# Performance work log

Hardware: AMD Instinct MI355X
Metric: run time of the kernel (lower is better)

Reference implementation:

```python
import jax, jax.numpy as jnp
import numpy as np
from jax import lax

B, C, DM, NL, NROI, HID, RHID, REMB = 2, 32, 64, 4, 90, 64, 64, 32
S = DM * DM * DM
EPS = 1e-5
DN = ('NCDHW', 'OIDHW', 'NCDHW')


def setup_inputs() -> dict:
    key = jax.random.key(0)
    ks = jax.random.split(key, 14)
    w = lambda k, shp, s=0.05: (jax.random.normal(k, shp, jnp.float32) * s)
    atlas = (jax.random.uniform(ks[1], (NROI, S)) < 0.1).astype(jnp.float32)
    return {
        'data': jax.random.normal(ks[0], (B, 1, DM, DM, DM), jnp.float32),
        'atlas_mask': atlas,
        'conv0_w': w(ks[2], (C, 1, 3, 3, 3), 0.2),
        'conv0_b': w(ks[3], (C,)),
        'convs_w': w(ks[4], (NL - 1, C, C, 3, 3, 3)),
        'convs_b': w(ks[5], (NL - 1, C)),
        'scale_w1': w(ks[6], (NROI, C, HID)),
        'scale_b1': w(ks[7], (NROI, HID)),
        'scale_w2': w(ks[8], (NROI, HID, C)),
        'scale_b2': w(ks[9], (NROI, C)),
        'proj_w1': w(ks[10], (NROI, C, RHID)),
        'proj_b1': w(ks[11], (NROI, RHID)),
        'proj_w2': w(ks[12], (NROI, RHID, REMB)),
        'proj_b2': w(ks[13], (NROI, REMB)),
    }


def _inorm(x):
    # InstanceNorm3d(affine=False): normalize per (batch, channel) over spatial dims
    m = jnp.mean(x, axis=(2, 3, 4), keepdims=True)
    v = jnp.var(x, axis=(2, 3, 4), keepdims=True)
    return (x - m) * lax.rsqrt(v + EPS)


def _conv(x, w, b):
    y = lax.conv_general_dilated(x, w, (1, 1, 1), 'SAME', dimension_numbers=DN)
    return y + b[None, :, None, None, None]


def reference(data, atlas_mask, conv0_w, conv0_b, convs_w, convs_b,
              scale_w1, scale_b1, scale_w2, scale_b2,
              proj_w1, proj_b1, proj_w2, proj_b2):
    x = jax.nn.relu(_inorm(_conv(data, conv0_w, conv0_b)))
    for i in range(NL - 1):  # fixed small layer loop
        x = jax.nn.relu(_inorm(_conv(x, convs_w[i], convs_b[i])))
    emb = x.reshape(B, C, S)                                  # (B,C,S)
    # (B,C,S) x (S,n_roi) -> (B,n_roi,C), normalized by ROI voxel count
    roi = jnp.einsum('bcs,rs->brc', emb, atlas_mask)
    roi = roi / atlas_mask.sum(axis=-1)[None, :, None]
    # per-ROI gated MLP experts, batched over the roi axis
    h = jax.nn.relu(jnp.einsum('brc,rch->brh', roi, scale_w1) + scale_b1[None])
    gate = jax.nn.sigmoid(jnp.einsum('brh,rhc->brc', h, scale_w2) + scale_b2[None])
    f = gate * roi
    p = jax.nn.relu(jnp.einsum('brc,rch->brh', f, proj_w1) + proj_b1[None])
    out = jnp.einsum('brh,rhe->bre', p, proj_w2) + proj_b2[None]
    return out  # (B, n_roi, roi_emb)
```

## Files before the change

### kernel.cpp

```cpp
#include <hip/hip_runtime.h>
#include <hip/hip_bf16.h>
#include <math.h>

#define S_TOT 262144
#define EPS_F 1e-5f
#define NPART 512
#define PLSTR 14416

typedef __attribute__((ext_vector_type(8))) short s16x8;
typedef __attribute__((ext_vector_type(4))) float f32x4;
typedef __attribute__((ext_vector_type(4))) unsigned u32x4;

__device__ __forceinline__ unsigned short f2bf(float f) {
    unsigned u = __builtin_bit_cast(unsigned, f);
    unsigned r = (u + 0x7FFFu + ((u >> 16) & 1u)) >> 16;
    return (unsigned short)r;
}
__device__ __forceinline__ float bf2f(unsigned short u) {
    return __builtin_bit_cast(float, ((unsigned)u) << 16);
}
__device__ __forceinline__ unsigned cvt_pk_bf16(float a, float b) {
    unsigned r;
    asm("v_cvt_pk_bf16_f32 %0, %1, %2" : "=v"(r) : "v"(a), "v"(b));
    return r;
}

__global__ __launch_bounds__(256)
void prep_w_k(const float* __restrict__ conv0_w, const float* __restrict__ convs_w,
              unsigned short* __restrict__ wpad, unsigned short* __restrict__ whp)
{
    int idx = blockIdx.x * 256 + threadIdx.x;
    if (idx < 2048) {
        int brow = idx >> 5, k = idx & 31;
        int cout = 2 * (brow & 15) + (brow >> 4);
        float wv = (k < 27) ? conv0_w[cout * 27 + k] : 0.f;
        unsigned short hi = f2bf(wv);
        unsigned short lo = f2bf(wv - bf2f(hi));
        wpad[brow * 32 + k]        = hi;
        wpad[1024 + brow * 32 + k] = lo;
        return;
    }
    int j = idx - 2048;
    if (j >= 3 * 27648) return;
    int layer = j / 27648 + 1;
    int rem   = j % 27648;
    int tap   = rem >> 10;
    int cout  = (rem >> 5) & 31;
    int cin   = rem & 31;
    float wv = convs_w[(((layer - 1) * 32 + cout) * 32 + cin) * 27 + tap];
    unsigned short hi = f2bf(wv);
    int brow = ((cout & 1) << 4) | (cout >> 1);
    whp[(size_t)(layer - 1) * 27648 + tap * 1024 + brow * 32 + cin] = hi;
}

__global__ __launch_bounds__(512, 2)
void conv0_k(const float* __restrict__ in, const unsigned short* __restrict__ w0,
             unsigned short* __restrict__ outb, float* __restrict__ raw_out)
{
    __shared__ unsigned short sc[1824];
    __shared__ float s_red[512];

    const int tid  = threadIdx.x;
    const int lane = tid & 63;
    const int wv   = tid >> 6;
    const int row  = lane & 15;
    const int g4   = lane >> 4;

    const int blk = blockIdx.x;
    const int b   = blk >> 8;
    const int t   = blk & 255;
    const int x0  = (t & 7) << 3;
    const int y0  = ((t >> 3) & 7) << 3;
    const int z0  = (t >> 6) << 4;

    for (int i = tid; i < 1800; i += 512) {
        int zz = i / 100, r2 = i - zz * 100, yy = r2 / 10, xx = r2 - yy * 10;
        int gz = z0 + zz - 1, gy = y0 + yy - 1, gx = x0 + xx - 1;
        float v = 0.f;
        if ((unsigned)gz < 64u && (unsigned)gy < 64u && (unsigned)gx < 64u)
            v = in[((size_t)b << 18) + (gz << 12) + (gy << 6) + gx];
        sc[i] = (unsigned short)cvt_pk_bf16(v, v);
    }
    __syncthreads();

    int dvox[8];
    #pragma unroll
    for (int j = 0; j < 8; ++j) {
        int tap = g4 * 8 + j;
        if (tap < 27) {
            int dz = tap / 9, r9 = tap - dz * 9, dy = r9 / 3, dx = r9 - dy * 3;
            dvox[j] = dz * 100 + dy * 10 + dx;
        } else dvox[j] = 0;
    }

    s16x8 wh0 = *(const s16x8*)(w0 + row * 32 + g4 * 8);
    s16x8 wh1 = *(const s16x8*)(w0 + (16 + row) * 32 + g4 * 8);
    s16x8 wl0 = *(const s16x8*)(w0 + 1024 + row * 32 + g4 * 8);
    s16x8 wl1 = *(const s16x8*)(w0 + 1024 + (16 + row) * 32 + g4 * 8);

    f32x4 acc[2][4][2] = {};
    #pragma unroll
    for (int pl = 0; pl < 2; ++pl) {
        #pragma unroll
        for (int f = 0; f < 4; ++f) {
            int vvx = f * 16 + row;
            int base = (2 * wv + pl) * 100 + (vvx >> 3) * 10 + (vvx & 7);
            s16x8 a;
            #pragma unroll
            for (int j = 0; j < 8; ++j) a[j] = (short)sc[base + dvox[j]];
            acc[pl][f][0] = __builtin_amdgcn_mfma_f32_16x16x32_bf16(a, wh0, acc[pl][f][0], 0, 0, 0);
            acc[pl][f][0] = __builtin_amdgcn_mfma_f32_16x16x32_bf16(a, wl0, acc[pl][f][0], 0, 0, 0);
            acc[pl][f][1] = __builtin_amdgcn_mfma_f32_16x16x32_bf16(a, wh1, acc[pl][f][1], 0, 0, 0);
            acc[pl][f][1] = __builtin_amdgcn_mfma_f32_16x16x32_bf16(a, wl1, acc[pl][f][1], 0, 0, 0);
        }
    }

    {
        float s0 = 0.f, ss0 = 0.f, s1 = 0.f, ss1 = 0.f;
        #pragma unroll
        for (int pl = 0; pl < 2; ++pl)
            #pragma unroll
            for (int f = 0; f < 4; ++f)
                #pragma unroll
                for (int q = 0; q < 4; ++q) {
                    float v0 = acc[pl][f][0][q], v1 = acc[pl][f][1][q];
                    s0 += v0; ss0 += v0 * v0; s1 += v1; ss1 += v1 * v1;
                }
        s0 += __shfl_xor(s0, 16); s0 += __shfl_xor(s0, 32);
        ss0 += __shfl_xor(ss0, 16); ss0 += __shfl_xor(ss0, 32);
        s1 += __shfl_xor(s1, 16); s1 += __shfl_xor(s1, 32);
        ss1 += __shfl_xor(ss1, 16); ss1 += __shfl_xor(ss1, 32);
        if (lane < 16) {
            s_red[(wv * 32 + 2 * row) * 2]         = s0;
            s_red[(wv * 32 + 2 * row) * 2 + 1]     = ss0;
            s_red[(wv * 32 + 2 * row + 1) * 2]     = s1;
            s_red[(wv * 32 + 2 * row + 1) * 2 + 1] = ss1;
        }
    }

    #pragma unroll
    for (int pl = 0; pl < 2; ++pl) {
        int zp = 2 * wv + pl;
        unsigned short* ob = outb
            + ((((size_t)b << 18) + ((size_t)(z0 + zp) << 12) + (y0 << 6) + x0) << 5)
            + (row << 1);
        #pragma unroll
        for (int f = 0; f < 4; ++f) {
            #pragma unroll
            for (int qq = 0; qq < 4; ++qq) {
                int u = g4 * 4 + qq;
                int yy = f * 2 + (u >> 3), xx = u & 7;
                unsigned pk = cvt_pk_bf16(acc[pl][f][0][qq], acc[pl][f][1][qq]);
                *(unsigned*)(ob + ((yy << 6) + xx) * 32) = pk;
            }
        }
    }

    __syncthreads();
    if (tid < 64) {
        int n = tid & 31, sel = tid >> 5;
        float tot = 0.f;
        #pragma unroll
        for (int w = 0; w < 8; ++w) tot += s_red[(w * 32 + n) * 2 + sel];
        atomicAdd(&raw_out[(b * 32 + n) * 2 + sel], tot);
    }
}

__global__ __launch_bounds__(1024, 4)
void conv_slab_k(const unsigned short* __restrict__ in, const unsigned short* __restrict__ whp_l,
                 const float* __restrict__ raw_in, unsigned short* __restrict__ outb,
                 float* __restrict__ raw_out)
{
    __shared__ unsigned short tile[4 * PLSTR];
    __shared__ float s_red[1024];

    const int tid  = threadIdx.x;
    const int lane = tid & 63;
    const int wv   = tid >> 6;
    const int zz   = wv >> 1;
    const int yh   = (wv & 1) << 2;
    const int row  = lane & 15;
    const int g4   = lane >> 4;
    const int g    = tid & 3;
    const int vox0 = tid >> 2;

    const int blk = blockIdx.x;
    const int b   = blk >> 8;
    const int t   = blk & 255;
    const int x0  = (t & 3) << 4;
    const int y0  = ((t >> 2) & 7) << 3;
    const int z0  = (t >> 5) << 3;

    {
        float rs[8], sh[8];
        #pragma unroll
        for (int j = 0; j < 8; ++j) {
            int c = b * 32 + g * 8 + j;
            float sm = raw_in[c * 2], sq = raw_in[c * 2 + 1];
            float mean = sm * (1.f / 262144.f);
            float var  = sq * (1.f / 262144.f) - mean * mean;
            float r = rsqrtf(var + EPS_F);
            rs[j] = r; sh[j] = -mean * r;
        }
        #pragma unroll 1
        for (int u = 0; u < 8; ++u) {
            int vox = vox0 + u * 256;
            if (vox >= 1800) break;
            int zp = vox / 180, r2 = vox - zp * 180, yy = r2 / 18, xx = r2 - yy * 18;
            int gz = z0 + zp - 1, gy = y0 + yy - 1, gx = x0 + xx - 1;
            u32x4 w = (u32x4)0;
            if ((unsigned)gz < 64u && (unsigned)gy < 64u && (unsigned)gx < 64u) {
                u32x4 rv = *(const u32x4*)(in
                    + ((((size_t)b << 18) + (gz << 12) + (gy << 6) + gx) << 5) + (g << 3));
                #pragma unroll
                for (int k = 0; k < 4; ++k) {
                    float ve = __builtin_bit_cast(float, rv[k] << 16);
                    float vo = __builtin_bit_cast(float, rv[k] & 0xFFFF0000u);
                    float ne = fmaxf(0.f, fmaf(ve, rs[2 * k],     sh[2 * k]));
                    float no = fmaxf(0.f, fmaf(vo, rs[2 * k + 1], sh[2 * k + 1]));
                    w[k] = cvt_pk_bf16(ne, no);
                }
            }
            *(u32x4*)&tile[g * PLSTR + (vox << 3)] = w;
        }
    }
    __syncthreads();

    f32x4 acc[4][2] = {};
    {
        const unsigned short* aplane = &tile[g4 * PLSTR];
        const unsigned short* wrow = whp_l + row * 32 + g4 * 8;

        #pragma unroll 1
        for (int dz = 0; dz < 3; ++dz) {
            #pragma unroll 1
            for (int dx = 0; dx < 3; ++dx) {
                const int base = (((zz + dz) * 180 + yh * 18 + row + dx) << 3);
                s16x8 a6[6];
                #pragma unroll
                for (int r6 = 0; r6 < 6; ++r6)
                    a6[r6] = *(const s16x8*)&aplane[base + r6 * 144];

                #pragma unroll
                for (int dy = 0; dy < 3; ++dy) {
                    const int tap = (dz * 3 + dy) * 3 + dx;
                    s16x8 w0v = *(const s16x8*)(wrow + tap * 1024);
                    s16x8 w1v = *(const s16x8*)(wrow + tap * 1024 + 512);
                    __builtin_amdgcn_s_setprio(1);
                    acc[0][0] = __builtin_amdgcn_mfma_f32_16x16x32_bf16(a6[dy],     w0v, acc[0][0], 0, 0, 0);
                    acc[1][0] = __builtin_amdgcn_mfma_f32_16x16x32_bf16(a6[dy + 1], w0v, acc[1][0], 0, 0, 0);
                    acc[2][0] = __builtin_amdgcn_mfma_f32_16x16x32_bf16(a6[dy + 2], w0v, acc[2][0], 0, 0, 0);
                    acc[3][0] = __builtin_amdgcn_mfma_f32_16x16x32_bf16(a6[dy + 3], w0v, acc[3][0], 0, 0, 0);
                    acc[0][1] = __builtin_amdgcn_mfma_f32_16x16x32_bf16(a6[dy],     w1v, acc[0][1], 0, 0, 0);
                    acc[1][1] = __builtin_amdgcn_mfma_f32_16x16x32_bf16(a6[dy + 1], w1v, acc[1][1], 0, 0, 0);
                    acc[2][1] = __builtin_amdgcn_mfma_f32_16x16x32_bf16(a6[dy + 2], w1v, acc[2][1], 0, 0, 0);
                    acc[3][1] = __builtin_amdgcn_mfma_f32_16x16x32_bf16(a6[dy + 3], w1v, acc[3][1], 0, 0, 0);
                    __builtin_amdgcn_s_setprio(0);
                }
            }
        }
    }

    {
        float s0 = 0.f, ss0 = 0.f, s1 = 0.f, ss1 = 0.f;
        #pragma unroll
        for (int fr = 0; fr < 4; ++fr)
            #pragma unroll
            for (int q = 0; q < 4; ++q) {
                float v0 = acc[fr][0][q], v1 = acc[fr][1][q];
                s0 += v0; ss0 += v0 * v0; s1 += v1; ss1 += v1 * v1;
            }
        s0 += __shfl_xor(s0, 16); s0 += __shfl_xor(s0, 32);
        ss0 += __shfl_xor(ss0, 16); ss0 += __shfl_xor(ss0, 32);
        s1 += __shfl_xor(s1, 16); s1 += __shfl_xor(s1, 32);
        ss1 += __shfl_xor(ss1, 16); ss1 += __shfl_xor(ss1, 32);
        if (lane < 16) {
            s_red[(wv * 32 + 2 * row) * 2]         = s0;
            s_red[(wv * 32 + 2 * row) * 2 + 1]     = ss0;
            s_red[(wv * 32 + 2 * row + 1) * 2]     = s1;
            s_red[(wv * 32 + 2 * row + 1) * 2 + 1] = ss1;
        }
    }

    #pragma unroll
    for (int fr = 0; fr < 4; ++fr) {
        unsigned short* ob = outb
            + ((((size_t)b << 18) + ((size_t)(z0 + zz) << 12) + ((y0 + yh + fr) << 6) + x0) << 5)
            + (row << 1);
        #pragma unroll
        for (int qq = 0; qq < 4; ++qq) {
            unsigned pk = cvt_pk_bf16(acc[fr][0][qq], acc[fr][1][qq]);
            *(unsigned*)(ob + ((g4 * 4 + qq) << 5)) = pk;
        }
    }

    __syncthreads();
    if (tid < 64) {
        int n = tid & 31, sel = tid >> 5;
        float tot = 0.f;
        #pragma unroll
        for (int w = 0; w < 16; ++w) tot += s_red[(w * 32 + n) * 2 + sel];
        atomicAdd(&raw_out[(b * 32 + n) * 2 + sel], tot);
    }
}

__global__ __launch_bounds__(256)
void pool_mfma_k(const unsigned short* __restrict__ emb, const float* __restrict__ raw3,
                 const float* __restrict__ mask, float* __restrict__ part,
                 float* __restrict__ cntp)
{
    __shared__ unsigned short Ald[64 * 136];
    __shared__ unsigned short Bld[96 * 136];
    __shared__ float s_ns[128];

    const int tid  = threadIdx.x;
    const int lane = tid & 63, wv = tid >> 6;
    const int row  = lane & 15, g4 = lane >> 4;

    if (tid < 64) {
        float sm = raw3[tid * 2], sq = raw3[tid * 2 + 1];
        float mean = sm * (1.f / 262144.f);
        float var  = sq * (1.f / 262144.f) - mean * mean;
        float r = rsqrtf(var + EPS_F);
        s_ns[tid]      = r;
        s_ns[64 + tid] = -mean * r;
    }

    f32x4 acc[6] = {};
    float csum[6] = {};

    for (int ch = 0; ch < 4; ++ch) {
        const int s0 = (blockIdx.x * 4 + ch) << 7;
        __syncthreads();
        for (int i = tid; i < 1024; i += 256) {
            int bb = i >> 9, v = (i >> 2) & 127, g = i & 3;
            u32x4 rv = *(const u32x4*)(emb + (((size_t)bb << 18) + (size_t)(s0 + v)) * 32 + (g << 3));
            #pragma unroll
            for (int k = 0; k < 4; ++k) {
                int bc = bb * 32 + (g << 3) + 2 * k;
                float ve = __builtin_bit_cast(float, rv[k] << 16);
                float vo = __builtin_bit_cast(float, rv[k] & 0xFFFF0000u);
                float ne = fmaxf(0.f, fmaf(ve, s_ns[bc],     s_ns[64 + bc]));
                float no = fmaxf(0.f, fmaf(vo, s_ns[bc + 1], s_ns[64 + bc + 1]));
                unsigned pk = cvt_pk_bf16(ne, no);
                Ald[bc * 136 + v]       = (unsigned short)pk;
                Ald[(bc + 1) * 136 + v] = (unsigned short)(pk >> 16);
            }
        }
        #pragma unroll
        for (int k = 0; k < 6; ++k) {
            int i = tid + k * 256;
            int r = i >> 4, bs = i & 15;
            s16x8 vec = (s16x8)0;
            if (r < 90) {
                const float* mp = mask + (size_t)r * S_TOT + s0 + bs * 8;
                float4 m0 = *(const float4*)mp;
                float4 m1 = *(const float4*)(mp + 4);
                vec[0] = (m0.x != 0.f) ? (short)0x3F80 : (short)0;
                vec[1] = (m0.y != 0.f) ? (short)0x3F80 : (short)0;
                vec[2] = (m0.z != 0.f) ? (short)0x3F80 : (short)0;
                vec[3] = (m0.w != 0.f) ? (short)0x3F80 : (short)0;
                vec[4] = (m1.x != 0.f) ? (short)0x3F80 : (short)0;
                vec[5] = (m1.y != 0.f) ? (short)0x3F80 : (short)0;
                vec[6] = (m1.z != 0.f) ? (short)0x3F80 : (short)0;
                vec[7] = (m1.w != 0.f) ? (short)0x3F80 : (short)0;
                csum[k] += m0.x + m0.y + m0.z + m0.w + m1.x + m1.y + m1.z + m1.w;
            }
            *(s16x8*)&Bld[r * 136 + bs * 8] = vec;
        }
        __syncthreads();
        #pragma unroll
        for (int kk = 0; kk < 4; ++kk) {
            s16x8 a = *(const s16x8*)&Ald[(wv * 16 + row) * 136 + kk * 32 + g4 * 8];
            #pragma unroll
            for (int j = 0; j < 6; ++j) {
                s16x8 bb = *(const s16x8*)&Bld[(j * 16 + row) * 136 + kk * 32 + g4 * 8];
                acc[j] = __builtin_amdgcn_mfma_f32_16x16x32_bf16(a, bb, acc[j], 0, 0, 0);
            }
        }
    }
    #pragma unroll
    for (int k = 0; k < 6; ++k) {
        float c = csum[k];
        c += __shfl_xor(c, 1); c += __shfl_xor(c, 2);
        c += __shfl_xor(c, 4); c += __shfl_xor(c, 8);
        if ((tid & 15) == 0)
            cntp[(size_t)blockIdx.x * 96 + (tid >> 4) + k * 16] = c;
    }
    #pragma unroll
    for (int j = 0; j < 6; ++j) {
        *(f32x4*)&part[((size_t)blockIdx.x * 96 + j * 16 + row) * 64 + wv * 16 + g4 * 4]
            = acc[j];
    }
}

__global__ __launch_bounds__(256)
void mlp_k(const float* __restrict__ part, const float* __restrict__ cntp,
           const float* __restrict__ w1, const float* __restrict__ b1,
           const float* __restrict__ w2, const float* __restrict__ b2,
           const float* __restrict__ pw1, const float* __restrict__ pb1,
           const float* __restrict__ pw2, const float* __restrict__ pb2,
           float* __restrict__ out)
{
    const int r   = blockIdx.x % 90;
    const int b   = blockIdx.x / 90;
    const int tid = threadIdx.x;
    __shared__ float sred[8 * 32];
    __shared__ float scnt[4];
    __shared__ float roi_s[32], h_s[64], f_s[32], p_s[64];

    {
        float csp = 0.f;
        for (int p = tid; p < NPART; p += 256) csp += cntp[(size_t)p * 96 + r];
        #pragma unroll
        for (int off = 32; off > 0; off >>= 1) csp += __shfl_xor(csp, off);
        if ((tid & 63) == 0) scnt[tid >> 6] = csp;
    }
    {
        const int c = tid & 31, seg = tid >> 5;
        const float* pp = part + ((size_t)(seg * (NPART / 8)) * 96 + r) * 64 + b * 32 + c;
        float s = 0.f;
        #pragma unroll 4
        for (int p = 0; p < NPART / 8; ++p) s += pp[(size_t)p * 6144];
        sred[seg * 32 + c] = s;
    }
    __syncthreads();
    if (tid < 32) {
        float cs = scnt[0] + scnt[1] + scnt[2] + scnt[3];
        float t = 0.f;
        #pragma unroll
        for (int k = 0; k < 8; ++k) t += sred[k * 32 + tid];
        roi_s[tid] = t / cs;
    }
    __syncthreads();
    if (tid < 64) {
        float s = b1[r * 64 + tid];
        for (int c = 0; c < 32; ++c)
            s = fmaf(roi_s[c], w1[(r * 32 + c) * 64 + tid], s);
        h_s[tid] = fmaxf(s, 0.f);
    }
    __syncthreads();
    if (tid < 32) {
        float s = b2[r * 32 + tid];
        for (int j = 0; j < 64; ++j)
            s = fmaf(h_s[j], w2[(r * 64 + j) * 32 + tid], s);
        float gate = 1.f / (1.f + expf(-s));
        f_s[tid] = gate * roi_s[tid];
    }
    __syncthreads();
    if (tid < 64) {
        float s = pb1[r * 64 + tid];
        for (int c = 0; c < 32; ++c)
            s = fmaf(f_s[c], pw1[(r * 32 + c) * 64 + tid], s);
        p_s[tid] = fmaxf(s, 0.f);
    }
    __syncthreads();
    if (tid < 32) {
        float s = pb2[r * 32 + tid];
        for (int j = 0; j < 64; ++j)
            s = fmaf(p_s[j], pw2[(r * 64 + j) * 32 + tid], s);
        out[((size_t)b * 90 + r) * 32 + tid] = s;
    }
}

extern "C" void kernel_launch(void* const* d_in, const int* in_sizes, int n_in,
                              void* d_out, int out_size, void* d_ws, size_t ws_size,
                              hipStream_t stream)
{
    const float* data    = (const float*)d_in[0];
    const float* mask    = (const float*)d_in[1];
    const float* conv0_w = (const float*)d_in[2];
    const float* convs_w = (const float*)d_in[4];
    const float* sw1 = (const float*)d_in[6];
    const float* sb1 = (const float*)d_in[7];
    const float* sw2 = (const float*)d_in[8];
    const float* sb2 = (const float*)d_in[9];
    const float* pw1 = (const float*)d_in[10];
    const float* pb1 = (const float*)d_in[11];
    const float* pw2 = (const float*)d_in[12];
    const float* pb2 = (const float*)d_in[13];
    float* out = (float*)d_out;

    float* ws = (float*)d_ws;
    unsigned short* bufA = (unsigned short*)ws;
    unsigned short* bufB = (unsigned short*)(ws + 8388608);
    unsigned short* wpad = (unsigned short*)(ws + 16777216);
    unsigned short* whp  = (unsigned short*)(ws + 16887808);
    float* raw   = ws + 16929280;
    float* part  = ws + 17825792;
    float* cntp  = part + 3145728;

    hipMemsetAsync(raw, 0, 512 * sizeof(float), stream);
    prep_w_k<<<332, 256, 0, stream>>>(conv0_w, convs_w, wpad, whp);

    conv0_k<<<512, 512, 0, stream>>>(data, wpad, bufA, raw);
    conv_slab_k<<<512, 1024, 0, stream>>>(bufA, whp, raw, bufB, raw + 128);
    conv_slab_k<<<512, 1024, 0, stream>>>(bufB, whp + 27648, raw + 128, bufA, raw + 256);
    conv_slab_k<<<512, 1024, 0, stream>>>(bufA, whp + 2 * 27648, raw + 256, bufB, raw + 384);

    pool_mfma_k<<<NPART, 256, 0, stream>>>(bufB, raw + 384, mask, part, cntp);

    mlp_k<<<180, 256, 0, stream>>>(part, cntp, sw1, sb1, sw2, sb2,
                                   pw1, pb1, pw2, pb2, out);
}
```

Before: 214.2 us.

## Split conv slab into two double-buffered half tiles with load/compute overlap

Each conv block now processes two smaller 8x4x16 tiles instead of one 8x8x16 tile. The global loads for the second tile are issued into registers before the first tile's MFMA work and committed to a second LDS buffer afterwards. The goal is to hide global-load latency behind compute. The cost is a larger halo fraction, which means more redundant loads and LDS writes, plus fewer accumulators per wave and extra register pressure from the pending prefetch.

```diff
diff --git a/kernel.cpp b/kernel.cpp
--- a/kernel.cpp
+++ b/kernel.cpp
@@ -5,7 +5,7 @@
 #define S_TOT 262144
 #define EPS_F 1e-5f
 #define NPART 512
-#define PLSTR 14416
+#define PL    8656
 
 typedef __attribute__((ext_vector_type(8))) short s16x8;
 typedef __attribute__((ext_vector_type(4))) float f32x4;
@@ -167,18 +167,17 @@
 }
 
 __global__ __launch_bounds__(1024, 4)
-void conv_slab_k(const unsigned short* __restrict__ in, const unsigned short* __restrict__ whp_l,
+void conv_pipe_k(const unsigned short* __restrict__ in, const unsigned short* __restrict__ whp_l,
                  const float* __restrict__ raw_in, unsigned short* __restrict__ outb,
                  float* __restrict__ raw_out)
 {
-    __shared__ unsigned short tile[4 * PLSTR];
-    __shared__ float s_red[1024];
+    __shared__ unsigned short buf[2][4 * PL];
 
     const int tid  = threadIdx.x;
     const int lane = tid & 63;
     const int wv   = tid >> 6;
     const int zz   = wv >> 1;
-    const int yh   = (wv & 1) << 2;
+    const int yp   = (wv & 1) << 1;
     const int row  = lane & 15;
     const int g4   = lane >> 4;
     const int g    = tid & 3;
@@ -186,114 +185,134 @@
 
     const int blk = blockIdx.x;
     const int b   = blk >> 8;
-    const int t   = blk & 255;
-    const int x0  = (t & 3) << 4;
-    const int y0  = ((t >> 2) & 7) << 3;
-    const int z0  = (t >> 5) << 3;
-
-    {
-        float rs[8], sh[8];
-        #pragma unroll
-        for (int j = 0; j < 8; ++j) {
-            int c = b * 32 + g * 8 + j;
-            float sm = raw_in[c * 2], sq = raw_in[c * 2 + 1];
-            float mean = sm * (1.f / 262144.f);
-            float var  = sq * (1.f / 262144.f) - mean * mean;
-            float r = rsqrtf(var + EPS_F);
-            rs[j] = r; sh[j] = -mean * r;
-        }
-        #pragma unroll 1
-        for (int u = 0; u < 8; ++u) {
+    const int j   = blk & 255;
+
+    float rs[8], sh[8];
+    #pragma unroll
+    for (int k = 0; k < 8; ++k) {
+        int c = b * 32 + g * 8 + k;
+        float sm = raw_in[c * 2], sq = raw_in[c * 2 + 1];
+        float mean = sm * (1.f / 262144.f);
+        float var  = sq * (1.f / 262144.f) - mean * mean;
+        float r = rsqrtf(var + EPS_F);
+        rs[k] = r; sh[k] = -mean * r;
+    }
+
+    u32x4 pend[5];
+    int   okm = 0;
+
+    auto issue = [&](int t) {
+        int x0t = (t & 3) << 4, y0t = ((t >> 2) & 15) << 2, z0t = (t >> 6) << 3;
+        okm = 0;
+        #pragma unroll
+        for (int u = 0; u < 5; ++u) {
             int vox = vox0 + u * 256;
-            if (vox >= 1800) break;
-            int zp = vox / 180, r2 = vox - zp * 180, yy = r2 / 18, xx = r2 - yy * 18;
-            int gz = z0 + zp - 1, gy = y0 + yy - 1, gx = x0 + xx - 1;
+            int zp = vox / 108, r2 = vox - zp * 108, yy = r2 / 18, xx = r2 - yy * 18;
+            int gz = z0t + zp - 1, gy = y0t + yy - 1, gx = x0t + xx - 1;
+            bool ok = (vox < 1080) && ((unsigned)gz < 64u) && ((unsigned)gy < 64u)
+                      && ((unsigned)gx < 64u);
+            okm |= ((int)ok) << u;
+            u32x4 v = (u32x4)0;
+            if (ok)
+                v = *(const u32x4*)(in
+                    + ((((size_t)b << 18) + (gz << 12) + (gy << 6) + gx) << 5) + (g << 3));
+            pend[u] = v;
+        }
+    };
+
+    auto commit = [&](unsigned short* bp) {
+        #pragma unroll
+        for (int u = 0; u < 5; ++u) {
+            int vox = vox0 + u * 256;
+            if (vox >= 1080) continue;
             u32x4 w = (u32x4)0;
-            if ((unsigned)gz < 64u && (unsigned)gy < 64u && (unsigned)gx < 64u) {
-                u32x4 rv = *(const u32x4*)(in
-                    + ((((size_t)b << 18) + (gz << 12) + (gy << 6) + gx) << 5) + (g << 3));
+            if ((okm >> u) & 1) {
                 #pragma unroll
                 for (int k = 0; k < 4; ++k) {
-                    float ve = __builtin_bit_cast(float, rv[k] << 16);
-                    float vo = __builtin_bit_cast(float, rv[k] & 0xFFFF0000u);
+                    float ve = __builtin_bit_cast(float, pend[u][k] << 16);
+                    float vo = __builtin_bit_cast(float, pend[u][k] & 0xFFFF0000u);
                     float ne = fmaxf(0.f, fmaf(ve, rs[2 * k],     sh[2 * k]));
                     float no = fmaxf(0.f, fmaf(vo, rs[2 * k + 1], sh[2 * k + 1]));
                     w[k] = cvt_pk_bf16(ne, no);
                 }
             }
-            *(u32x4*)&tile[g * PLSTR + (vox << 3)] = w;
-        }
-    }
-    __syncthreads();
-
-    f32x4 acc[4][2] = {};
-    {
-        const unsigned short* aplane = &tile[g4 * PLSTR];
-        const unsigned short* wrow = whp_l + row * 32 + g4 * 8;
-
+            *(u32x4*)&bp[g * PL + (vox << 3)] = w;
+        }
+    };
+
+    const unsigned short* wrow = whp_l + row * 32 + g4 * 8;
+    float s0 = 0.f, ss0 = 0.f, s1 = 0.f, ss1 = 0.f;
+    f32x4 acc[2][2];
+
+    auto tile_compute = [&](const unsigned short* bp, int t) {
+        acc[0][0] = (f32x4)0.f; acc[0][1] = (f32x4)0.f;
+        acc[1][0] = (f32x4)0.f; acc[1][1] = (f32x4)0.f;
+        const unsigned short* aplane = bp + g4 * PL;
         #pragma unroll 1
         for (int dz = 0; dz < 3; ++dz) {
             #pragma unroll 1
             for (int dx = 0; dx < 3; ++dx) {
-                const int base = (((zz + dz) * 180 + yh * 18 + row + dx) << 3);
-                s16x8 a6[6];
+                const int base = (((zz + dz) * 108 + yp * 18 + row + dx) << 3);
+                s16x8 a4[4];
                 #pragma unroll
-                for (int r6 = 0; r6 < 6; ++r6)
-                    a6[r6] = *(const s16x8*)&aplane[base + r6 * 144];
-
+                for (int r4 = 0; r4 < 4; ++r4)
+                    a4[r4] = *(const s16x8*)&aplane[base + r4 * 144];
                 #pragma unroll
                 for (int dy = 0; dy < 3; ++dy) {
                     const int tap = (dz * 3 + dy) * 3 + dx;
                     s16x8 w0v = *(const s16x8*)(wrow + tap * 1024);
                     s16x8 w1v = *(const s16x8*)(wrow + tap * 1024 + 512);
                     __builtin_amdgcn_s_setprio(1);
-                    acc[0][0] = __builtin_amdgcn_mfma_f32_16x16x32_bf16(a6[dy],     w0v, acc[0][0], 0, 0, 0);
-                    acc[1][0] = __builtin_amdgcn_mfma_f32_16x16x32_bf16(a6[dy + 1], w0v, acc[1][0], 0, 0, 0);
-                    acc[2][0] = __builtin_amdgcn_mfma_f32_16x16x32_bf16(a6[dy + 2], w0v, acc[2][0], 0, 0, 0);
-                    acc[3][0] = __builtin_amdgcn_mfma_f32_16x16x32_bf16(a6[dy + 3], w0v, acc[3][0], 0, 0, 0);
-                    acc[0][1] = __builtin_amdgcn_mfma_f32_16x16x32_bf16(a6[dy],     w1v, acc[0][1], 0, 0, 0);
-                    acc[1][1] = __builtin_amdgcn_mfma_f32_16x16x32_bf16(a6[dy + 1], w1v, acc[1][1], 0, 0, 0);
-                    acc[2][1] = __builtin_amdgcn_mfma_f32_16x16x32_bf16(a6[dy + 2], w1v, acc[2][1], 0, 0, 0);
-                    acc[3][1] = __builtin_amdgcn_mfma_f32_16x16x32_bf16(a6[dy + 3], w1v, acc[3][1], 0, 0, 0);
+                    acc[0][0] = __builtin_amdgcn_mfma_f32_16x16x32_bf16(a4[dy],     w0v, acc[0][0], 0, 0, 0);
+                    acc[1][0] = __builtin_amdgcn_mfma_f32_16x16x32_bf16(a4[dy + 1], w0v, acc[1][0], 0, 0, 0);
+                    acc[0][1] = __builtin_amdgcn_mfma_f32_16x16x32_bf16(a4[dy],     w1v, acc[0][1], 0, 0, 0);
+                    acc[1][1] = __builtin_amdgcn_mfma_f32_16x16x32_bf16(a4[dy + 1], w1v, acc[1][1], 0, 0, 0);
                     __builtin_amdgcn_s_setprio(0);
                 }
             }
         }
-    }
-
-    {
-        float s0 = 0.f, ss0 = 0.f, s1 = 0.f, ss1 = 0.f;
-        #pragma unroll
-        for (int fr = 0; fr < 4; ++fr)
+        #pragma unroll
+        for (int fr = 0; fr < 2; ++fr)
             #pragma unroll
             for (int q = 0; q < 4; ++q) {
                 float v0 = acc[fr][0][q], v1 = acc[fr][1][q];
                 s0 += v0; ss0 += v0 * v0; s1 += v1; ss1 += v1 * v1;
             }
-        s0 += __shfl_xor(s0, 16); s0 += __shfl_xor(s0, 32);
-        ss0 += __shfl_xor(ss0, 16); ss0 += __shfl_xor(ss0, 32);
-        s1 += __shfl_xor(s1, 16); s1 += __shfl_xor(s1, 32);
-        ss1 += __shfl_xor(ss1, 16); ss1 += __shfl_xor(ss1, 32);
-        if (lane < 16) {
-            s_red[(wv * 32 + 2 * row) * 2]         = s0;
-            s_red[(wv * 32 + 2 * row) * 2 + 1]     = ss0;
-            s_red[(wv * 32 + 2 * row + 1) * 2]     = s1;
-            s_red[(wv * 32 + 2 * row + 1) * 2 + 1] = ss1;
-        }
-    }
-
-    #pragma unroll
-    for (int fr = 0; fr < 4; ++fr) {
-        unsigned short* ob = outb
-            + ((((size_t)b << 18) + ((size_t)(z0 + zz) << 12) + ((y0 + yh + fr) << 6) + x0) << 5)
-            + (row << 1);
-        #pragma unroll
-        for (int qq = 0; qq < 4; ++qq) {
-            unsigned pk = cvt_pk_bf16(acc[fr][0][qq], acc[fr][1][qq]);
-            *(unsigned*)(ob + ((g4 * 4 + qq) << 5)) = pk;
-        }
-    }
-
+        int x0t = (t & 3) << 4, y0t = ((t >> 2) & 15) << 2, z0t = (t >> 6) << 3;
+        #pragma unroll
+        for (int fr = 0; fr < 2; ++fr) {
+            unsigned short* ob = outb
+                + ((((size_t)b << 18) + ((size_t)(z0t + zz) << 12)
+                  + ((y0t + yp + fr) << 6) + x0t) << 5) + (row << 1);
+            #pragma unroll
+            for (int qq = 0; qq < 4; ++qq) {
+                unsigned pk = cvt_pk_bf16(acc[fr][0][qq], acc[fr][1][qq]);
+                *(unsigned*)(ob + ((g4 * 4 + qq) << 5)) = pk;
+            }
+        }
+    };
+
+    const int t0 = 2 * j, t1 = 2 * j + 1;
+    issue(t0);
+    commit(buf[0]);
+    __syncthreads();
+    issue(t1);
+    tile_compute(buf[0], t0);
+    commit(buf[1]);
+    __syncthreads();
+    tile_compute(buf[1], t1);
+
+    float* s_red = (float*)&buf[0][0];
+    s0 += __shfl_xor(s0, 16); s0 += __shfl_xor(s0, 32);
+    ss0 += __shfl_xor(ss0, 16); ss0 += __shfl_xor(ss0, 32);
+    s1 += __shfl_xor(s1, 16); s1 += __shfl_xor(s1, 32);
+    ss1 += __shfl_xor(ss1, 16); ss1 += __shfl_xor(ss1, 32);
+    if (lane < 16) {
+        s_red[(wv * 32 + 2 * row) * 2]         = s0;
+        s_red[(wv * 32 + 2 * row) * 2 + 1]     = ss0;
+        s_red[(wv * 32 + 2 * row + 1) * 2]     = s1;
+        s_red[(wv * 32 + 2 * row + 1) * 2 + 1] = ss1;
+    }
     __syncthreads();
     if (tid < 64) {
         int n = tid & 31, sel = tid >> 5;
@@ -494,9 +513,9 @@
     prep_w_k<<<332, 256, 0, stream>>>(conv0_w, convs_w, wpad, whp);
 
     conv0_k<<<512, 512, 0, stream>>>(data, wpad, bufA, raw);
-    conv_slab_k<<<512, 1024, 0, stream>>>(bufA, whp, raw, bufB, raw + 128);
-    conv_slab_k<<<512, 1024, 0, stream>>>(bufB, whp + 27648, raw + 128, bufA, raw + 256);
-    conv_slab_k<<<512, 1024, 0, stream>>>(bufA, whp + 2 * 27648, raw + 256, bufB, raw + 384);
+    conv_pipe_k<<<512, 1024, 0, stream>>>(bufA, whp, raw, bufB, raw + 128);
+    conv_pipe_k<<<512, 1024, 0, stream>>>(bufB, whp + 27648, raw + 128, bufA, raw + 256);
+    conv_pipe_k<<<512, 1024, 0, stream>>>(bufA, whp + 2 * 27648, raw + 256, bufB, raw + 384);
 
     pool_mfma_k<<<NPART, 256, 0, stream>>>(bufB, raw + 384, mask, part, cntp);
 
```

After: 279.5 us. +30.5%, slower.
